# Optimization experiments

Measured on AMD Instinct MI355X. Metric: run time of the kernel, lower is better.

## Reference

```python
import jax, jax.numpy as jnp
import numpy as np

N = 4000; T_GRU = 32; T_TREE = 16; F = 256; HS = 128; H = 3 * HS; CC = 512; E = 64000; D4 = 4 * HS


def _gru_last(x, wi, wh, bi, bh):
    # x: [N, T, F]; torch GRU gate order r, z, n. Returns last hidden [N, H].
    xp = jnp.einsum('ntf,gf->ntg', x, wi) + bi  # [N, T, 3H]
    h0 = jnp.zeros((x.shape[0], wh.shape[1]), x.dtype)
    def step(h, xt):
        gh = h @ wh.T + bh
        ir, iz, inn = jnp.split(xt, 3, axis=1)
        hr, hz, hn = jnp.split(gh, 3, axis=1)
        r = jax.nn.sigmoid(ir + hr)
        z = jax.nn.sigmoid(iz + hz)
        n = jnp.tanh(inn + r * hn)
        return (1.0 - z) * n + z * h, None
    hT, _ = jax.lax.scan(step, h0, jnp.swapaxes(xp, 0, 1))
    return hT


def _tree_root(x, ioux_w, ioux_b, iouh_w, iouh_b, fx_w, fx_b, fh_w, fh_b):
    # Chain-structured TreeLSTM (each node has one child); x: [N, T, F], leaf-to-root.
    xi = jnp.einsum('ntf,gf->ntg', x, ioux_w) + ioux_b  # [N, T, 3M]
    xf = jnp.einsum('ntf,mf->ntm', x, fx_w) + fx_b      # [N, T, M]
    M = fh_w.shape[0]
    z0 = jnp.zeros((x.shape[0], M), x.dtype)
    def step(carry, xs):
        c, h = carry
        xi_t, xf_t = xs
        iou = xi_t + h @ iouh_w.T + iouh_b
        i, o, u = jnp.split(iou, 3, axis=1)
        f = jax.nn.sigmoid(xf_t + h @ fh_w.T + fh_b)
        c = jax.nn.sigmoid(i) * jnp.tanh(u) + f * c
        h = jax.nn.sigmoid(o) * jnp.tanh(c)
        return (c, h), None
    (c, h), _ = jax.lax.scan(step, (z0, z0), (jnp.swapaxes(xi, 0, 1), jnp.swapaxes(xf, 0, 1)))
    return h


def _gcn(x, w, b, row, col):
    # PyG GCNConv: self-loops + symmetric normalization.
    n = x.shape[0]
    xw = x @ w.T
    loops = jnp.arange(n, dtype=row.dtype)
    r = jnp.concatenate([row, loops])
    c = jnp.concatenate([col, loops])
    deg = jax.ops.segment_sum(jnp.ones(r.shape, x.dtype), c, num_segments=n)
    dinv = jnp.where(deg > 0, jax.lax.rsqrt(jnp.maximum(deg, 1e-12)), 0.0)
    norm = (dinv[r] * dinv[c])[:, None]
    return jax.ops.segment_sum(xw[r] * norm, c, num_segments=n) + b


def setup_inputs() -> dict:
    key = jax.random.key(0)
    ks = jax.random.split(key, 48)
    s = 0.05
    p = lambda i, sh: jax.random.normal(ks[i], sh, jnp.float32) * s
    return {
        'feat1': p(0, (N, T_GRU, F)),
        'feat2': p(1, (N, T_TREE, F)),
        'feat3': p(2, (N, T_TREE, F)),
        'feat4': p(3, (N, CC)),
        'edge_index': jax.random.randint(ks[4], (2, E), 0, N),
        'gru_wi': p(5, (3 * H, F)), 'gru_wh': p(6, (3 * H, H)),
        'gru_bi': p(7, (3 * H,)), 'gru_bh': p(8, (3 * H,)),
        't1_ioux_w': p(9, (3 * H, F)), 't1_ioux_b': p(10, (3 * H,)),
        't1_iouh_w': p(11, (3 * H, H)), 't1_iouh_b': p(12, (3 * H,)),
        't1_fx_w': p(13, (H, F)), 't1_fx_b': p(14, (H,)),
        't1_fh_w': p(15, (H, H)), 't1_fh_b': p(16, (H,)),
        't2_ioux_w': p(17, (3 * H, F)), 't2_ioux_b': p(18, (3 * H,)),
        't2_iouh_w': p(19, (3 * H, H)), 't2_iouh_b': p(20, (3 * H,)),
        't2_fx_w': p(21, (H, F)), 't2_fx_b': p(22, (H,)),
        't2_fh_w': p(23, (H, H)), 't2_fh_b': p(24, (H,)),
        'r1_w': p(25, (HS, H)), 'r1_b': p(26, (HS,)),
        'r2_w': p(27, (HS, H)), 'r2_b': p(28, (HS,)),
        'r3_w': p(29, (HS, H)), 'r3_b': p(30, (HS,)),
        'r4_w': p(31, (HS, CC)), 'r4_b': p(32, (HS,)),
        'gcn0_w': p(33, (D4, D4)), 'gcn0_b': p(34, (D4,)),
        'gcn1_w': p(35, (D4, D4)), 'gcn1_b': p(36, (D4,)),
        'r7_w': p(37, (2, D4)), 'r7_b': p(38, (2,)),
    }


def reference(feat1, feat2, feat3, feat4, edge_index,
              gru_wi, gru_wh, gru_bi, gru_bh,
              t1_ioux_w, t1_ioux_b, t1_iouh_w, t1_iouh_b, t1_fx_w, t1_fx_b, t1_fh_w, t1_fh_b,
              t2_ioux_w, t2_ioux_b, t2_iouh_w, t2_iouh_b, t2_fx_w, t2_fx_b, t2_fh_w, t2_fh_b,
              r1_w, r1_b, r2_w, r2_b, r3_w, r3_b, r4_w, r4_b,
              gcn0_w, gcn0_b, gcn1_w, gcn1_b, r7_w, r7_b):
    v1 = _gru_last(feat1, gru_wi, gru_wh, gru_bi, gru_bh)            # [N, H]
    v2 = _tree_root(feat2, t1_ioux_w, t1_ioux_b, t1_iouh_w, t1_iouh_b, t1_fx_w, t1_fx_b, t1_fh_w, t1_fh_b)
    v3 = _tree_root(feat3, t2_ioux_w, t2_ioux_b, t2_iouh_w, t2_iouh_b, t2_fx_w, t2_fx_b, t2_fh_w, t2_fh_b)
    f1 = v1 @ r1_w.T + r1_b
    f2 = v2 @ r2_w.T + r2_b
    f3 = v3 @ r3_w.T + r3_b
    f4 = feat4 @ r4_w.T + r4_b
    m = jnp.concatenate([f1, f2, f3, f4], axis=1)                    # [N, 4*HS]
    row, col = edge_index[0], edge_index[1]
    m = jax.nn.relu(_gcn(m, gcn0_w, gcn0_b, row, col))
    m = _gcn(m, gcn1_w, gcn1_b, row, col)
    m = jax.nn.softmax(m @ r7_w.T + r7_b, axis=1)                    # [N, 2]
    return m.T                                                       # [2, N]
```

## Files before the change

### kernel.cpp

```cpp
#include <hip/hip_runtime.h>
#include <hip/hip_bf16.h>
#include <math.h>

#define NN 4000
#define TG 32
#define TT 16
#define FF 256
#define HH 384
#define GCOLS 1536
#define KCAT 640
#define EE 64000
#define D4 512

typedef __attribute__((ext_vector_type(8))) short short8;
typedef __attribute__((ext_vector_type(4))) float float4v;

static __device__ __forceinline__ float fsig(float x)  { return 1.0f / (1.0f + __expf(-x)); }
static __device__ __forceinline__ float ftanh(float x) { return 2.0f / (1.0f + __expf(-2.0f*x)) - 1.0f; }
static __device__ __forceinline__ unsigned short f2bf(float f) {
    __hip_bfloat16 h = __float2bfloat16(f); return *reinterpret_cast<unsigned short*>(&h);
}

static __device__ __forceinline__ void async_copy16(const void* g, void* l) {
    __builtin_amdgcn_global_load_lds(
        (const __attribute__((address_space(1))) unsigned int*)g,
        (__attribute__((address_space(3))) unsigned int*)l, 16, 0, 0);
}

__global__ __launch_bounds__(256) void prep_w_kernel(
    const float* __restrict__ gwi, const float* __restrict__ gwh,
    const float* __restrict__ gbi, const float* __restrict__ gbh,
    const float* __restrict__ x1w, const float* __restrict__ x1b,
    const float* __restrict__ h1w, const float* __restrict__ h1b,
    const float* __restrict__ fx1w, const float* __restrict__ fx1b,
    const float* __restrict__ fh1w, const float* __restrict__ fh1b,
    const float* __restrict__ x2w, const float* __restrict__ x2b,
    const float* __restrict__ h2w, const float* __restrict__ h2b,
    const float* __restrict__ fx2w, const float* __restrict__ fx2b,
    const float* __restrict__ fh2w, const float* __restrict__ fh2b,
    __hip_bfloat16* __restrict__ Wx, __hip_bfloat16* __restrict__ Wh,
    float* __restrict__ bp)
{
    int z = blockIdx.z;
    int idx = blockIdx.x * 256 + threadIdx.x;
    int c = idx / KCAT, k = idx - c * KCAT;
    int bx = c >> 7, wc = (c >> 6) & 1, g = (c >> 4) & 3, rl = c & 15;
    int j = bx*32 + wc*16 + rl;
    float v = 0.0f, bv = 0.0f;
    if (z == 0) {
        if (g <= 1) {
            int row = g*HH + j;
            v = (k < FF) ? gwi[row*FF + k] : gwh[row*HH + (k-FF)];
            bv = gbi[row] + gbh[row];
        } else if (g == 2) {
            int row = 2*HH + j;
            v = (k < FF) ? gwi[row*FF + k] : 0.0f;
            bv = gbi[row];
        } else {
            int row = 2*HH + j;
            v = (k < FF) ? 0.0f : gwh[row*HH + (k-FF)];
            bv = gbh[row];
        }
    } else {
        const float* xw  = (z==1)? x1w  : x2w;   const float* xb  = (z==1)? x1b  : x2b;
        const float* hw  = (z==1)? h1w  : h2w;   const float* hb_ = (z==1)? h1b  : h2b;
        const float* fxw = (z==1)? fx1w : fx2w;  const float* fxb = (z==1)? fx1b : fx2b;
        const float* fhw = (z==1)? fh1w : fh2w;  const float* fhb = (z==1)? fh1b : fh2b;
        if (g < 3) {
            int row = g*HH + j;
            v = (k < FF) ? xw[row*FF + k] : hw[row*HH + (k-FF)];
            bv = xb[row] + hb_[row];
        } else {
            v = (k < FF) ? fxw[j*FF + k] : fhw[j*HH + (k-FF)];
            bv = fxb[j] + fhb[j];
        }
    }
    if (k < FF) Wx[(size_t)z*GCOLS*FF + (size_t)c*FF + k] = __float2bfloat16(v);
    else        Wh[(size_t)z*GCOLS*HH + (size_t)c*HH + (k-FF)] = __float2bfloat16(v);
    if (k == 0) bp[z*GCOLS + c] = bv;
}

__global__ __launch_bounds__(256) void f2b4_kernel(const float* __restrict__ s,
                                                   __hip_bfloat16* __restrict__ d, int n4)
{
    int i = blockIdx.x*256 + threadIdx.x;
    if (i >= n4) return;
    float4 v = ((const float4*)s)[i];
    ushort4 u = { f2bf(v.x), f2bf(v.y), f2bf(v.z), f2bf(v.w) };
    ((ushort4*)d)[i] = u;
}

#define BM 128
#define BN 128
#define BKK 32

__global__ __launch_bounds__(256) void gemm0_k(
    const __hip_bfloat16* __restrict__ Ab, size_t zA, int lda,
    const __hip_bfloat16* __restrict__ Wb, size_t zW, int K,
    const float* __restrict__ bias, size_t zB,
    float* __restrict__ C, size_t zC,
    __hip_bfloat16* __restrict__ C16, size_t zC16,
    int ldC, int M)
{
    const int z = blockIdx.z;
    const __hip_bfloat16* A = Ab + zA*z;
    const __hip_bfloat16* W = Wb + zW*z;

    __shared__ __align__(16) __hip_bfloat16 As[BM][BKK];
    __shared__ __align__(16) __hip_bfloat16 Bs[BN][BKK];

    const int tid  = threadIdx.x;
    const int lane = tid & 63;
    const int w    = tid >> 6;
    const int wr = w >> 1, wc = w & 1;
    const int rowBase = blockIdx.y * BM;
    const int colBase = blockIdx.x * BN;
    const int sRow = tid >> 2;
    const int sK   = (tid & 3) * 8;

    float4v acc[4][4];
    #pragma unroll
    for (int i = 0; i < 4; ++i)
        #pragma unroll
        for (int j = 0; j < 4; ++j)
            acc[i][j] = (float4v){0.f, 0.f, 0.f, 0.f};

    const int rl = lane & 15;
    const int kl = (lane >> 4) * 8;

    for (int kt = 0; kt < K; kt += BKK) {
        const int kk = kt + sK;
        #pragma unroll
        for (int i = 0; i < 2; ++i) {
            int gr = rowBase + i*64 + sRow;
            if (gr > M-1) gr = M-1;
            async_copy16(A + (size_t)gr*lda + kk, &As[i*64 + sRow][sK]);
        }
        #pragma unroll
        for (int i = 0; i < 2; ++i) {
            int r = i*64 + sRow;
            async_copy16(W + (size_t)(colBase + r)*K + kk, &Bs[r][sK]);
        }
        __syncthreads();

        short8 af[4], bfr[4];
        #pragma unroll
        for (int mi = 0; mi < 4; ++mi)
            af[mi] = *(const short8*)&As[wr*64 + mi*16 + rl][kl];
        #pragma unroll
        for (int ni = 0; ni < 4; ++ni)
            bfr[ni] = *(const short8*)&Bs[wc*64 + ni*16 + rl][kl];
        #pragma unroll
        for (int mi = 0; mi < 4; ++mi)
            #pragma unroll
            for (int ni = 0; ni < 4; ++ni)
                acc[mi][ni] = __builtin_amdgcn_mfma_f32_16x16x32_bf16(af[mi], bfr[ni], acc[mi][ni], 0, 0, 0);
        __syncthreads();
    }

    const int rq = (lane >> 4) * 4;
    float* Cz = C + zC*z;
    __hip_bfloat16* C16z = C16 ? (C16 + zC16*z) : nullptr;
    #pragma unroll
    for (int mi = 0; mi < 4; ++mi) {
        #pragma unroll
        for (int q = 0; q < 4; ++q) {
            int row = rowBase + wr*64 + mi*16 + rq + q;
            if (row >= M) continue;
            #pragma unroll
            for (int ni = 0; ni < 4; ++ni) {
                int col = colBase + wc*64 + ni*16 + rl;
                float v = acc[mi][ni][q];
                if (bias) v += bias[zB*z + col];
                Cz[(size_t)row*ldC + col] = v;
                if (C16z) C16z[(size_t)row*ldC + col] = __float2bfloat16(v);
            }
        }
    }
}

#define SBM 64

template<int MODE>
__global__ __launch_bounds__(256) void step_k(
    const __hip_bfloat16* __restrict__ Xb, size_t zX, int lda, int xoff,
    const __hip_bfloat16* __restrict__ Hin, size_t zH,
    const __hip_bfloat16* __restrict__ Wxb, size_t zWx,
    const __hip_bfloat16* __restrict__ Whb, size_t zWh,
    const float* __restrict__ bp, size_t zB,
    const float* __restrict__ Sin, size_t zS,
    float* __restrict__ Sout, size_t zSo,
    __hip_bfloat16* __restrict__ Hout, size_t zHo)
{
    const int z = blockIdx.z;
    const __hip_bfloat16* X  = Xb + zX*z;
    const __hip_bfloat16* Hi = Hin + zH*z;
    const __hip_bfloat16* Wx = Wxb + zWx*z;
    const __hip_bfloat16* Wh = Whb + zWh*z;
    const float* Si = Sin + zS*z;
    float* So = Sout + zSo*z;
    __hip_bfloat16* Ho = Hout + zHo*z;

    __shared__ __align__(16) __hip_bfloat16 As[2][SBM][BKK];
    __shared__ __align__(16) __hip_bfloat16 Bs[2][BN][BKK];

    const int tid  = threadIdx.x;
    const int lane = tid & 63;
    const int w    = tid >> 6;
    const int wr = w >> 1, wc = w & 1;
    const int rowBase = blockIdx.y * SBM;
    const int colBase = blockIdx.x * BN;
    const int sRow = tid >> 2;
    const int sK   = (tid & 3) * 8;

    int grA = rowBase + sRow; if (grA > NN-1) grA = NN-1;
    const int cB0 = colBase + sRow;
    const int cB1 = colBase + 64 + sRow;

    float4v acc[2][4];
    #pragma unroll
    for (int i = 0; i < 2; ++i)
        #pragma unroll
        for (int j = 0; j < 4; ++j)
            acc[i][j] = (float4v){0.f, 0.f, 0.f, 0.f};

    const int rl = lane & 15;
    const int kl = (lane >> 4) * 8;

    auto stage = [&](int buf, int kt) {
        const int kk = kt + sK;
        if (kk < FF) {
            async_copy16(X  + (size_t)grA*lda + xoff + kk, &As[buf][sRow][sK]);
            async_copy16(Wx + (size_t)cB0*FF + kk,         &Bs[buf][sRow][sK]);
            async_copy16(Wx + (size_t)cB1*FF + kk,         &Bs[buf][64 + sRow][sK]);
        } else {
            async_copy16(Hi + (size_t)grA*HH + (kk-FF),    &As[buf][sRow][sK]);
            async_copy16(Wh + (size_t)cB0*HH + (kk-FF),    &Bs[buf][sRow][sK]);
            async_copy16(Wh + (size_t)cB1*HH + (kk-FF),    &Bs[buf][64 + sRow][sK]);
        }
    };

    stage(0, 0);
    int cur = 0;
    for (int kt = 0; kt < KCAT; kt += BKK) {
        if (kt + BKK < KCAT) {
            stage(cur ^ 1, kt + BKK);
            asm volatile("s_waitcnt vmcnt(3)");
        } else {
            asm volatile("s_waitcnt vmcnt(0)");
        }
        __builtin_amdgcn_sched_barrier(0);
        __builtin_amdgcn_s_barrier();
        __builtin_amdgcn_sched_barrier(0);

        short8 af[2], bfr[4];
        #pragma unroll
        for (int mi = 0; mi < 2; ++mi)
            af[mi] = *(const short8*)&As[cur][wr*32 + mi*16 + rl][kl];

        if (MODE == 1 && kt < FF) {
            #pragma unroll
            for (int ni = 0; ni < 3; ++ni)
                bfr[ni] = *(const short8*)&Bs[cur][wc*64 + ni*16 + rl][kl];
            #pragma unroll
            for (int mi = 0; mi < 2; ++mi)
                #pragma unroll
                for (int ni = 0; ni < 3; ++ni)
                    acc[mi][ni] = __builtin_amdgcn_mfma_f32_16x16x32_bf16(af[mi], bfr[ni], acc[mi][ni], 0, 0, 0);
        } else if (MODE == 1) {
            bfr[0] = *(const short8*)&Bs[cur][wc*64 + 0*16 + rl][kl];
            bfr[1] = *(const short8*)&Bs[cur][wc*64 + 1*16 + rl][kl];
            bfr[3] = *(const short8*)&Bs[cur][wc*64 + 3*16 + rl][kl];
            #pragma unroll
            for (int mi = 0; mi < 2; ++mi) {
                acc[mi][0] = __builtin_amdgcn_mfma_f32_16x16x32_bf16(af[mi], bfr[0], acc[mi][0], 0, 0, 0);
                acc[mi][1] = __builtin_amdgcn_mfma_f32_16x16x32_bf16(af[mi], bfr[1], acc[mi][1], 0, 0, 0);
                acc[mi][3] = __builtin_amdgcn_mfma_f32_16x16x32_bf16(af[mi], bfr[3], acc[mi][3], 0, 0, 0);
            }
        } else {
            #pragma unroll
            for (int ni = 0; ni < 4; ++ni)
                bfr[ni] = *(const short8*)&Bs[cur][wc*64 + ni*16 + rl][kl];
            #pragma unroll
            for (int mi = 0; mi < 2; ++mi)
                #pragma unroll
                for (int ni = 0; ni < 4; ++ni)
                    acc[mi][ni] = __builtin_amdgcn_mfma_f32_16x16x32_bf16(af[mi], bfr[ni], acc[mi][ni], 0, 0, 0);
        }
        __builtin_amdgcn_sched_barrier(0);
        __builtin_amdgcn_s_barrier();
        cur ^= 1;
    }

    const int rq = (lane >> 4) * 4;
    const int j  = (colBase >> 2) + wc*16 + rl;
    const int cb = colBase + wc*64 + rl;
    float b0 = bp[zB*z + cb + 0];
    float b1 = bp[zB*z + cb + 16];
    float b2 = bp[zB*z + cb + 32];
    float b3 = bp[zB*z + cb + 48];

    #pragma unroll
    for (int mi = 0; mi < 2; ++mi) {
        #pragma unroll
        for (int q = 0; q < 4; ++q) {
            int row = rowBase + wr*32 + mi*16 + rq + q;
            if (row >= NN) continue;
            float g0 = acc[mi][0][q] + b0;
            float g1 = acc[mi][1][q] + b1;
            float g2 = acc[mi][2][q] + b2;
            float g3 = acc[mi][3][q] + b3;
            size_t off = (size_t)row*HH + j;
            if (MODE == 1) {
                float r  = fsig(g0), zz = fsig(g1);
                float n  = ftanh(g2 + r*g3);
                float hp = Si[off];
                float hn = (1.0f - zz)*n + zz*hp;
                So[off] = hn;
                Ho[off] = __float2bfloat16(hn);
            } else {
                float cp = Si[off];
                float cn = fsig(g0)*ftanh(g2) + fsig(g3)*cp;
                So[off] = cn;
                float hn = fsig(g1)*ftanh(cn);
                Ho[off] = __float2bfloat16(hn);
            }
        }
    }
}

__global__ __launch_bounds__(256) void count_kernel(const int* __restrict__ col, int* __restrict__ degi)
{
    int e = blockIdx.x*256 + threadIdx.x;
    if (e < EE) atomicAdd(&degi[col[e]], 1);
}

__global__ __launch_bounds__(1024) void scan_kernel(const int* __restrict__ degi,
    int* __restrict__ start, int* __restrict__ cursor, float* __restrict__ dinv)
{
    __shared__ int s[1024];
    int t = threadIdx.x;
    int v[4]; int sum = 0;
    #pragma unroll
    for (int i = 0; i < 4; ++i) {
        int idx = t*4 + i;
        v[i] = (idx < NN) ? degi[idx] : 0;
        sum += v[i];
    }
    s[t] = sum;
    __syncthreads();
    for (int d = 1; d < 1024; d <<= 1) {
        int x = (t >= d) ? s[t-d] : 0;
        __syncthreads();
        s[t] += x;
        __syncthreads();
    }
    int base = s[t] - sum;
    int run = 0;
    #pragma unroll
    for (int i = 0; i < 4; ++i) {
        int idx = t*4 + i;
        if (idx < NN) {
            int st = base + run;
            start[idx] = st;
            cursor[idx] = st;
            dinv[idx] = rsqrtf((float)v[i] + 1.0f);
        }
        run += v[i];
    }
    if (t == 1023) start[NN] = s[1023];
}

__global__ __launch_bounds__(256) void fill_kernel(const int* __restrict__ row,
    const int* __restrict__ col, int* __restrict__ cursor, int* __restrict__ esrc)
{
    int e = blockIdx.x*256 + threadIdx.x;
    if (e < EE) {
        int c = col[e];
        int pos = atomicAdd(&cursor[c], 1);
        esrc[pos] = row[e];
    }
}

__global__ __launch_bounds__(256) void gather_kernel(const float* __restrict__ xw,
    const int* __restrict__ esrc, const int* __restrict__ start,
    const float* __restrict__ dinv, const float* __restrict__ bias,
    float* __restrict__ mout, __hip_bfloat16* __restrict__ mout16, int relu)
{
    int wv = threadIdx.x >> 6, lane = threadIdx.x & 63;
    int n = blockIdx.x*4 + wv;
    if (n >= NN) return;
    float a[8] = {0.f,0.f,0.f,0.f,0.f,0.f,0.f,0.f};
    int s0 = start[n], s1 = start[n+1];
    float dn = dinv[n];
    for (int e = s0; e < s1; ++e) {
        int r = esrc[e];
        float nrm = dinv[r]*dn;
        const float4 v0 = *(const float4*)(xw + (size_t)r*D4 + lane*8);
        const float4 v1 = *(const float4*)(xw + (size_t)r*D4 + lane*8 + 4);
        a[0] += v0.x*nrm; a[1] += v0.y*nrm; a[2] += v0.z*nrm; a[3] += v0.w*nrm;
        a[4] += v1.x*nrm; a[5] += v1.y*nrm; a[6] += v1.z*nrm; a[7] += v1.w*nrm;
    }
    const float4 u0 = *(const float4*)(xw + (size_t)n*D4 + lane*8);
    const float4 u1 = *(const float4*)(xw + (size_t)n*D4 + lane*8 + 4);
    float dd = dn*dn;
    float su[8] = {u0.x,u0.y,u0.z,u0.w,u1.x,u1.y,u1.z,u1.w};
    #pragma unroll
    for (int i = 0; i < 8; ++i) {
        float vv = a[i] + su[i]*dd + bias[lane*8 + i];
        if (relu) vv = fmaxf(vv, 0.0f);
        mout[(size_t)n*D4 + lane*8 + i] = vv;
        if (mout16) mout16[(size_t)n*D4 + lane*8 + i] = __float2bfloat16(vv);
    }
}

__global__ __launch_bounds__(256) void final_kernel(const float* __restrict__ m,
    const float* __restrict__ w, const float* __restrict__ b, float* __restrict__ out)
{
    int wave = threadIdx.x >> 6;
    int lane = threadIdx.x & 63;
    int n = blockIdx.x*4 + wave;
    const float* row = m + (size_t)n*D4 + lane*8;
    float4 v0 = *(const float4*)(row);
    float4 v1 = *(const float4*)(row + 4);
    const float* w0 = w + lane*8;
    const float* w1 = w + D4 + lane*8;
    float4 u0 = *(const float4*)(w0); float4 u1 = *(const float4*)(w0 + 4);
    float4 t0 = *(const float4*)(w1); float4 t1 = *(const float4*)(w1 + 4);
    float a = v0.x*u0.x + v0.y*u0.y + v0.z*u0.z + v0.w*u0.w
            + v1.x*u1.x + v1.y*u1.y + v1.z*u1.z + v1.w*u1.w;
    float bb = v0.x*t0.x + v0.y*t0.y + v0.z*t0.z + v0.w*t0.w
             + v1.x*t1.x + v1.y*t1.y + v1.z*t1.z + v1.w*t1.w;
    #pragma unroll
    for (int s = 32; s; s >>= 1) { a += __shfl_xor(a, s); bb += __shfl_xor(bb, s); }
    if (lane == 0) {
        float l0 = a + b[0], l1 = bb + b[1];
        float mx = fmaxf(l0, l1);
        float e0 = expf(l0 - mx), e1 = expf(l1 - mx);
        float s = e0 + e1;
        out[n]      = e0 / s;
        out[NN + n] = e1 / s;
    }
}

extern "C" void kernel_launch(void* const* d_in, const int* in_sizes, int n_in,
                              void* d_out, int out_size, void* d_ws, size_t ws_size,
                              hipStream_t stream)
{
    const float* feat1 = (const float*)d_in[0];
    const float* feat2 = (const float*)d_in[1];
    const float* feat3 = (const float*)d_in[2];
    const float* feat4 = (const float*)d_in[3];
    const int*   eidx  = (const int*)d_in[4];
    const float* r1w = (const float*)d_in[25]; const float* r1b = (const float*)d_in[26];
    const float* r2w = (const float*)d_in[27]; const float* r2b = (const float*)d_in[28];
    const float* r3w = (const float*)d_in[29]; const float* r3b = (const float*)d_in[30];
    const float* r4w = (const float*)d_in[31]; const float* r4b = (const float*)d_in[32];
    const float* g0w = (const float*)d_in[33]; const float* g0b = (const float*)d_in[34];
    const float* g1w = (const float*)d_in[35]; const float* g1b = (const float*)d_in[36];
    const float* r7w = (const float*)d_in[37]; const float* r7b = (const float*)d_in[38];

    float* ws = (float*)d_ws;
    size_t o = 0;
    auto alloc = [&](size_t nfl) { float* p = ws + o; o += (nfl + 3) & ~(size_t)3; return p; };

    float* hf0 = alloc((size_t)NN*HH);
    float* cf0 = alloc((size_t)2*NN*HH);
    __hip_bfloat16* hb0 = (__hip_bfloat16*)alloc((size_t)3*NN*HH/2);
    size_t zeroFloats = o;
    float* hf1 = alloc((size_t)NN*HH);
    float* cf1 = alloc((size_t)2*NN*HH);
    __hip_bfloat16* hb1 = (__hip_bfloat16*)alloc((size_t)3*NN*HH/2);
    __hip_bfloat16* xg  = (__hip_bfloat16*)alloc((size_t)TG*NN*FF/2);
    __hip_bfloat16* xt  = (__hip_bfloat16*)alloc((size_t)2*TT*NN*FF/2);
    __hip_bfloat16* Wx  = (__hip_bfloat16*)alloc((size_t)3*GCOLS*FF/2);
    __hip_bfloat16* Wh  = (__hip_bfloat16*)alloc((size_t)3*GCOLS*HH/2);
    float* bp   = alloc(3*GCOLS);
    float* mbuf = alloc((size_t)NN*D4);
    float* xwb  = alloc((size_t)NN*D4);
    float* dinv = alloc(NN);
    __hip_bfloat16* mbf16 = (__hip_bfloat16*)alloc((size_t)NN*D4/2);
    __hip_bfloat16* f4b   = (__hip_bfloat16*)alloc((size_t)NN*D4/2);
    __hip_bfloat16* rw123 = (__hip_bfloat16*)alloc((size_t)3*128*HH/2);
    float* rb123 = alloc(3*128);
    __hip_bfloat16* r4w16 = (__hip_bfloat16*)alloc((size_t)128*D4/2);
    __hip_bfloat16* g0w16 = (__hip_bfloat16*)alloc((size_t)D4*D4/2);
    __hip_bfloat16* g1w16 = (__hip_bfloat16*)alloc((size_t)D4*D4/2);
    int* degi   = (int*)alloc(NN);
    int* start  = (int*)alloc(NN + 4);
    int* cursor = (int*)alloc(NN);
    int* esrc   = (int*)alloc(EE);

    float* hfp[2] = {hf0, hf1};
    float* cfp[2] = {cf0, cf1};
    __hip_bfloat16* hbp[2] = {hb0, hb1};

    hipMemsetAsync(hf0, 0, zeroFloats*sizeof(float), stream);
    hipMemsetAsync(degi, 0, NN*sizeof(int), stream);

    prep_w_kernel<<<dim3(3840,1,3),256,0,stream>>>(
        (const float*)d_in[5],(const float*)d_in[6],(const float*)d_in[7],(const float*)d_in[8],
        (const float*)d_in[9],(const float*)d_in[10],(const float*)d_in[11],(const float*)d_in[12],
        (const float*)d_in[13],(const float*)d_in[14],(const float*)d_in[15],(const float*)d_in[16],
        (const float*)d_in[17],(const float*)d_in[18],(const float*)d_in[19],(const float*)d_in[20],
        (const float*)d_in[21],(const float*)d_in[22],(const float*)d_in[23],(const float*)d_in[24],
        Wx, Wh, bp);

    f2b4_kernel<<<32000,256,0,stream>>>(feat1, xg, TG*NN*FF/4);
    f2b4_kernel<<<16000,256,0,stream>>>(feat2, xt, TT*NN*FF/4);
    f2b4_kernel<<<16000,256,0,stream>>>(feat3, xt + (size_t)TT*NN*FF, TT*NN*FF/4);
    f2b4_kernel<<<2000,256,0,stream>>>(feat4, f4b, NN*D4/4);
    f2b4_kernel<<<48,256,0,stream>>>(r1w, rw123, 128*HH/4);
    f2b4_kernel<<<48,256,0,stream>>>(r2w, rw123 + 128*HH, 128*HH/4);
    f2b4_kernel<<<48,256,0,stream>>>(r3w, rw123 + 2*128*HH, 128*HH/4);
    f2b4_kernel<<<64,256,0,stream>>>(r4w, r4w16, 128*D4/4);
    f2b4_kernel<<<256,256,0,stream>>>(g0w, g0w16, D4*D4/4);
    f2b4_kernel<<<256,256,0,stream>>>(g1w, g1w16, D4*D4/4);
    hipMemcpyAsync(rb123,       r1b, 128*sizeof(float), hipMemcpyDeviceToDevice, stream);
    hipMemcpyAsync(rb123 + 128, r2b, 128*sizeof(float), hipMemcpyDeviceToDevice, stream);
    hipMemcpyAsync(rb123 + 256, r3b, 128*sizeof(float), hipMemcpyDeviceToDevice, stream);

    count_kernel<<<250,256,0,stream>>>(eidx + EE, degi);
    scan_kernel<<<1,1024,0,stream>>>(degi, start, cursor, dinv);
    fill_kernel<<<250,256,0,stream>>>(eidx, eidx + EE, cursor, esrc);

    for (int t = 0; t < TG; ++t) {
        int p = t & 1, q = p ^ 1;
        step_k<1><<<dim3(GCOLS/BN, 63, 1),256,0,stream>>>(
            xg, 0, TG*FF, t*FF,
            hbp[p], 0,
            Wx, 0, Wh, 0,
            bp, 0,
            hfp[p], 0, hfp[q], 0, hbp[q], 0);
    }
    for (int t = 0; t < TT; ++t) {
        int p = t & 1, q = p ^ 1;
        step_k<2><<<dim3(GCOLS/BN, 63, 2),256,0,stream>>>(
            xt, (size_t)TT*NN*FF, TT*FF, t*FF,
            hbp[p] + (size_t)NN*HH, (size_t)NN*HH,
            Wx + (size_t)GCOLS*FF, (size_t)GCOLS*FF,
            Wh + (size_t)GCOLS*HH, (size_t)GCOLS*HH,
            bp + GCOLS, GCOLS,
            cfp[p], (size_t)NN*HH, cfp[q], (size_t)NN*HH,
            hbp[q] + (size_t)NN*HH, (size_t)NN*HH);
    }

    gemm0_k<<<dim3(1,32,3),256,0,stream>>>(
        hbp[0], (size_t)NN*HH, HH, rw123, (size_t)128*HH, HH, rb123, 128,
        mbuf, 128, mbf16, 128, D4, NN);
    gemm0_k<<<dim3(1,32,1),256,0,stream>>>(
        f4b, 0, D4, r4w16, 0, D4, r4b, 0,
        mbuf + 384, 0, mbf16 + 384, 0, D4, NN);

    gemm0_k<<<dim3(4,32,1),256,0,stream>>>(
        mbf16, 0, D4, g0w16, 0, D4, nullptr, 0,
        xwb, 0, nullptr, 0, D4, NN);
    gather_kernel<<<1000,256,0,stream>>>(xwb, esrc, start, dinv, g0b, mbuf, mbf16, 1);

    gemm0_k<<<dim3(4,32,1),256,0,stream>>>(
        mbf16, 0, D4, g1w16, 0, D4, nullptr, 0,
        xwb, 0, nullptr, 0, D4, NN);
    gather_kernel<<<1000,256,0,stream>>>(xwb, esrc, start, dinv, g1b, mbuf, nullptr, 0);

    final_kernel<<<1000,256,0,stream>>>(mbuf, r7w, r7b, (float*)d_out);
}
```

Baseline: 1.559 ms.

## Fuse GRU and TreeLSTM step launches, add LDS swizzle and deeper prefetch

The first 16 GRU timesteps now run in the same launch as the two TreeLSTM steps, selected by blockIdx.z. That cuts the kernel launch count and fills the GPU with a larger grid. The step kernel's LDS tiles are XOR-swizzled to reduce bank conflicts. A 4-buffer ring that prefetches two tiles ahead replaces the double buffer and drops one barrier per iteration. The costs are more shared memory per block and branch divergence on mode at run time.

Result: no change. 1.589 ms (+1.9%).

```diff
diff --git a/kernel.cpp b/kernel.cpp
--- a/kernel.cpp
+++ b/kernel.cpp
@@ -180,29 +180,36 @@
 }
 
 #define SBM 64
+#define NT (KCAT/BKK)
+
+struct StepSet {
+    const __hip_bfloat16 *X, *Hin, *Wx, *Wh;
+    const float *bp, *Sin;
+    float *Sout;
+    __hip_bfloat16 *Hout;
+    int lda, xoff;
+};
 
 template<int MODE>
-__global__ __launch_bounds__(256) void step_k(
-    const __hip_bfloat16* __restrict__ Xb, size_t zX, int lda, int xoff,
-    const __hip_bfloat16* __restrict__ Hin, size_t zH,
-    const __hip_bfloat16* __restrict__ Wxb, size_t zWx,
-    const __hip_bfloat16* __restrict__ Whb, size_t zWh,
-    const float* __restrict__ bp, size_t zB,
-    const float* __restrict__ Sin, size_t zS,
-    float* __restrict__ Sout, size_t zSo,
-    __hip_bfloat16* __restrict__ Hout, size_t zHo)
-{
-    const int z = blockIdx.z;
-    const __hip_bfloat16* X  = Xb + zX*z;
-    const __hip_bfloat16* Hi = Hin + zH*z;
-    const __hip_bfloat16* Wx = Wxb + zWx*z;
-    const __hip_bfloat16* Wh = Whb + zWh*z;
-    const float* Si = Sin + zS*z;
-    float* So = Sout + zSo*z;
-    __hip_bfloat16* Ho = Hout + zHo*z;
-
-    __shared__ __align__(16) __hip_bfloat16 As[2][SBM][BKK];
-    __shared__ __align__(16) __hip_bfloat16 Bs[2][BN][BKK];
+__global__ __launch_bounds__(256) void step_k(StepSet G, StepSet T)
+{
+    int mode, zt;
+    if (MODE == 3 && blockIdx.z > 0) { mode = 2; zt = blockIdx.z - 1; }
+    else { mode = 1; zt = 0; }
+    const StepSet& S = (mode == 1) ? G : T;
+
+    const __hip_bfloat16* X  = S.X   + (size_t)zt*TT*NN*FF;
+    const __hip_bfloat16* Hi = S.Hin + (size_t)zt*NN*HH;
+    const __hip_bfloat16* Wx = S.Wx  + (size_t)zt*GCOLS*FF;
+    const __hip_bfloat16* Wh = S.Wh  + (size_t)zt*GCOLS*HH;
+    const float* bp = S.bp + (size_t)zt*GCOLS;
+    const float* Si = S.Sin + (size_t)zt*NN*HH;
+    float* So = S.Sout + (size_t)zt*NN*HH;
+    __hip_bfloat16* Ho = S.Hout + (size_t)zt*NN*HH;
+    const int lda = S.lda, xoff = S.xoff;
+
+    __shared__ __align__(16) __hip_bfloat16 As[4][SBM][BKK];
+    __shared__ __align__(16) __hip_bfloat16 Bs[4][BN][BKK];
 
     const int tid  = threadIdx.x;
     const int lane = tid & 63;
@@ -210,12 +217,25 @@
     const int wr = w >> 1, wc = w & 1;
     const int rowBase = blockIdx.y * SBM;
     const int colBase = blockIdx.x * BN;
-    const int sRow = tid >> 2;
-    const int sK   = (tid & 3) * 8;
-
-    int grA = rowBase + sRow; if (grA > NN-1) grA = NN-1;
-    const int cB0 = colBase + sRow;
-    const int cB1 = colBase + 64 + sRow;
+
+    const int sR  = tid >> 2;
+    const int sC  = tid & 3;
+    const int sSw = sC ^ ((sR >> 1) & 3);
+    int gra = rowBase + sR; if (gra > NN-1) gra = NN-1;
+
+    auto stage = [&](int buf, int kt) {
+        if (kt < FF) {
+            const int kk = kt + sSw*8;
+            async_copy16(X  + (size_t)gra*lda + xoff + kk,          &As[buf][sR][sC*8]);
+            async_copy16(Wx + (size_t)(colBase + sR)*FF + kk,       &Bs[buf][sR][sC*8]);
+            async_copy16(Wx + (size_t)(colBase + 64 + sR)*FF + kk,  &Bs[buf][64 + sR][sC*8]);
+        } else {
+            const int kk = kt - FF + sSw*8;
+            async_copy16(Hi + (size_t)gra*HH + kk,                  &As[buf][sR][sC*8]);
+            async_copy16(Wh + (size_t)(colBase + sR)*HH + kk,       &Bs[buf][sR][sC*8]);
+            async_copy16(Wh + (size_t)(colBase + 64 + sR)*HH + kk,  &Bs[buf][64 + sR][sC*8]);
+        }
+    };
 
     float4v acc[2][4];
     #pragma unroll
@@ -225,80 +245,71 @@
             acc[i][j] = (float4v){0.f, 0.f, 0.f, 0.f};
 
     const int rl = lane & 15;
-    const int kl = (lane >> 4) * 8;
-
-    auto stage = [&](int buf, int kt) {
-        const int kk = kt + sK;
-        if (kk < FF) {
-            async_copy16(X  + (size_t)grA*lda + xoff + kk, &As[buf][sRow][sK]);
-            async_copy16(Wx + (size_t)cB0*FF + kk,         &Bs[buf][sRow][sK]);
-            async_copy16(Wx + (size_t)cB1*FF + kk,         &Bs[buf][64 + sRow][sK]);
-        } else {
-            async_copy16(Hi + (size_t)grA*HH + (kk-FF),    &As[buf][sRow][sK]);
-            async_copy16(Wh + (size_t)cB0*HH + (kk-FF),    &Bs[buf][sRow][sK]);
-            async_copy16(Wh + (size_t)cB1*HH + (kk-FF),    &Bs[buf][64 + sRow][sK]);
-        }
-    };
+    const int dF = (lane >> 4) ^ ((rl >> 1) & 3);
 
     stage(0, 0);
-    int cur = 0;
-    for (int kt = 0; kt < KCAT; kt += BKK) {
-        if (kt + BKK < KCAT) {
-            stage(cur ^ 1, kt + BKK);
-            asm volatile("s_waitcnt vmcnt(3)");
-        } else {
-            asm volatile("s_waitcnt vmcnt(0)");
-        }
+    stage(1, BKK);
+
+    for (int it = 0; it < NT; ++it) {
+        if (it < NT-1) asm volatile("s_waitcnt vmcnt(3)" ::: "memory");
+        else           asm volatile("s_waitcnt vmcnt(0)" ::: "memory");
         __builtin_amdgcn_sched_barrier(0);
         __builtin_amdgcn_s_barrier();
         __builtin_amdgcn_sched_barrier(0);
-
+        if (it + 2 < NT) stage((it+2)&3, (it+2)*BKK);
+        __builtin_amdgcn_sched_barrier(0);
+
+        const int cur = it & 3;
         short8 af[2], bfr[4];
         #pragma unroll
         for (int mi = 0; mi < 2; ++mi)
-            af[mi] = *(const short8*)&As[cur][wr*32 + mi*16 + rl][kl];
-
-        if (MODE == 1 && kt < FF) {
+            af[mi] = *(const short8*)&As[cur][wr*32 + mi*16 + rl][dF*8];
+
+        const bool xph = (it*BKK) < FF;
+        if (mode == 2) {
+            #pragma unroll
+            for (int ni = 0; ni < 4; ++ni)
+                bfr[ni] = *(const short8*)&Bs[cur][wc*64 + ni*16 + rl][dF*8];
+            asm volatile("s_waitcnt lgkmcnt(0)" ::: "memory");
+            __builtin_amdgcn_sched_barrier(0);
+            #pragma unroll
+            for (int mi = 0; mi < 2; ++mi)
+                #pragma unroll
+                for (int ni = 0; ni < 4; ++ni)
+                    acc[mi][ni] = __builtin_amdgcn_mfma_f32_16x16x32_bf16(af[mi], bfr[ni], acc[mi][ni], 0, 0, 0);
+        } else if (xph) {
             #pragma unroll
             for (int ni = 0; ni < 3; ++ni)
-                bfr[ni] = *(const short8*)&Bs[cur][wc*64 + ni*16 + rl][kl];
+                bfr[ni] = *(const short8*)&Bs[cur][wc*64 + ni*16 + rl][dF*8];
+            asm volatile("s_waitcnt lgkmcnt(0)" ::: "memory");
+            __builtin_amdgcn_sched_barrier(0);
             #pragma unroll
             for (int mi = 0; mi < 2; ++mi)
                 #pragma unroll
                 for (int ni = 0; ni < 3; ++ni)
                     acc[mi][ni] = __builtin_amdgcn_mfma_f32_16x16x32_bf16(af[mi], bfr[ni], acc[mi][ni], 0, 0, 0);
-        } else if (MODE == 1) {
-            bfr[0] = *(const short8*)&Bs[cur][wc*64 + 0*16 + rl][kl];
-            bfr[1] = *(const short8*)&Bs[cur][wc*64 + 1*16 + rl][kl];
-            bfr[3] = *(const short8*)&Bs[cur][wc*64 + 3*16 + rl][kl];
+        } else {
+            bfr[0] = *(const short8*)&Bs[cur][wc*64 + 0*16 + rl][dF*8];
+            bfr[1] = *(const short8*)&Bs[cur][wc*64 + 1*16 + rl][dF*8];
+            bfr[3] = *(const short8*)&Bs[cur][wc*64 + 3*16 + rl][dF*8];
+            asm volatile("s_waitcnt lgkmcnt(0)" ::: "memory");
+            __builtin_amdgcn_sched_barrier(0);
             #pragma unroll
             for (int mi = 0; mi < 2; ++mi) {
                 acc[mi][0] = __builtin_amdgcn_mfma_f32_16x16x32_bf16(af[mi], bfr[0], acc[mi][0], 0, 0, 0);
                 acc[mi][1] = __builtin_amdgcn_mfma_f32_16x16x32_bf16(af[mi], bfr[1], acc[mi][1], 0, 0, 0);
                 acc[mi][3] = __builtin_amdgcn_mfma_f32_16x16x32_bf16(af[mi], bfr[3], acc[mi][3], 0, 0, 0);
             }
-        } else {
-            #pragma unroll
-            for (int ni = 0; ni < 4; ++ni)
-                bfr[ni] = *(const short8*)&Bs[cur][wc*64 + ni*16 + rl][kl];
-            #pragma unroll
-            for (int mi = 0; mi < 2; ++mi)
-                #pragma unroll
-                for (int ni = 0; ni < 4; ++ni)
-                    acc[mi][ni] = __builtin_amdgcn_mfma_f32_16x16x32_bf16(af[mi], bfr[ni], acc[mi][ni], 0, 0, 0);
-        }
-        __builtin_amdgcn_sched_barrier(0);
-        __builtin_amdgcn_s_barrier();
-        cur ^= 1;
+        }
     }
 
     const int rq = (lane >> 4) * 4;
     const int j  = (colBase >> 2) + wc*16 + rl;
     const int cb = colBase + wc*64 + rl;
-    float b0 = bp[zB*z + cb + 0];
-    float b1 = bp[zB*z + cb + 16];
-    float b2 = bp[zB*z + cb + 32];
-    float b3 = bp[zB*z + cb + 48];
+    float b0 = bp[cb + 0];
+    float b1 = bp[cb + 16];
+    float b2 = bp[cb + 32];
+    float b3 = bp[cb + 48];
 
     #pragma unroll
     for (int mi = 0; mi < 2; ++mi) {
@@ -311,7 +322,7 @@
             float g2 = acc[mi][2][q] + b2;
             float g3 = acc[mi][3][q] + b3;
             size_t off = (size_t)row*HH + j;
-            if (MODE == 1) {
+            if (mode == 1) {
                 float r  = fsig(g0), zz = fsig(g1);
                 float n  = ftanh(g2 + r*g3);
                 float hp = Si[off];
@@ -524,25 +535,19 @@
     scan_kernel<<<1,1024,0,stream>>>(degi, start, cursor, dinv);
     fill_kernel<<<250,256,0,stream>>>(eidx, eidx + EE, cursor, esrc);
 
-    for (int t = 0; t < TG; ++t) {
-        int p = t & 1, q = p ^ 1;
-        step_k<1><<<dim3(GCOLS/BN, 63, 1),256,0,stream>>>(
-            xg, 0, TG*FF, t*FF,
-            hbp[p], 0,
-            Wx, 0, Wh, 0,
-            bp, 0,
-            hfp[p], 0, hfp[q], 0, hbp[q], 0);
-    }
     for (int t = 0; t < TT; ++t) {
         int p = t & 1, q = p ^ 1;
-        step_k<2><<<dim3(GCOLS/BN, 63, 2),256,0,stream>>>(
-            xt, (size_t)TT*NN*FF, TT*FF, t*FF,
-            hbp[p] + (size_t)NN*HH, (size_t)NN*HH,
-            Wx + (size_t)GCOLS*FF, (size_t)GCOLS*FF,
-            Wh + (size_t)GCOLS*HH, (size_t)GCOLS*HH,
-            bp + GCOLS, GCOLS,
-            cfp[p], (size_t)NN*HH, cfp[q], (size_t)NN*HH,
-            hbp[q] + (size_t)NN*HH, (size_t)NN*HH);
+        StepSet Gs = { xg, hbp[p], Wx, Wh, bp, hfp[p], hfp[q], hbp[q], TG*FF, t*FF };
+        StepSet Ts = { xt, hbp[p] + (size_t)NN*HH,
+                       Wx + (size_t)GCOLS*FF, Wh + (size_t)GCOLS*HH,
+                       bp + GCOLS, cfp[p], cfp[q],
+                       hbp[q] + (size_t)NN*HH, TT*FF, t*FF };
+        step_k<3><<<dim3(GCOLS/BN, 63, 3),256,0,stream>>>(Gs, Ts);
+    }
+    for (int t = TT; t < TG; ++t) {
+        int p = t & 1, q = p ^ 1;
+        StepSet Gs = { xg, hbp[p], Wx, Wh, bp, hfp[p], hfp[q], hbp[q], TG*FF, t*FF };
+        step_k<1><<<dim3(GCOLS/BN, 63, 1),256,0,stream>>>(Gs, Gs);
     }
 
     gemm0_k<<<dim3(1,32,3),256,0,stream>>>(
```
